# Optimization experiments

Measured on AMD Instinct MI355X. Metric: run time of the kernel, lower is better.

Reference implementation:

```python
import jax, jax.numpy as jnp
import numpy as np

H, W = 512, 1024            # panorama resolution
GRID = 512                  # occupancy histogram resolution (height=width=512)
ABS_SCALE = 20000.0         # mm, ground-plane extent
UNIT_SCALE = 1000.0         # m -> mm
COUNT_TH = 100.0            # histogram count clamp


def _xyz_sphere(ref_plan):
    # Vectorized version of the original double loop.
    i = np.arange(H, dtype=np.float32)
    j = np.arange(W, dtype=np.float32)
    theta = -np.pi * (i / (H - 1) - 0.5)          # [H]
    phi = np.pi * (2.0 * j / (W - 1) - 1.0)       # [W]
    ct, st = np.cos(theta)[:, None], np.sin(theta)[:, None]   # [H,1]
    cp, sp = np.cos(phi)[None, :], np.sin(phi)[None, :]       # [1,W]
    if ref_plan == 'horizontal':
        P = np.stack([cp * ct, sp * ct, np.broadcast_to(st, (H, W))], 0)
    elif ref_plan == 'vertical':
        P = np.stack([cp * ct, np.broadcast_to(-st, (H, W)), sp * ct], 0)
    else:  # lateral
        P = np.stack([sp * ct, np.broadcast_to(-st, (H, W)), cp * ct], 0)
    return jnp.asarray(P.astype(np.float32))      # [3,H,W]

_SPHERES = [_xyz_sphere(p) for p in ('horizontal', 'vertical', 'lateral')]


def _density_one(depth_hw, sph):
    # depth_hw: [H,W]; sph: [3,H,W]
    ps = depth_hw[None] * sph                               # [3,H,W] 3D points
    xy = ps[:2].reshape(2, -1) * UNIT_SCALE                 # [2,N] mm, (x,y)
    coords = (xy + ABS_SCALE / 2.0) / ABS_SCALE * GRID      # [2,N] in grid units
    coords = jnp.clip(jnp.round(coords), 0.0, GRID - 1).astype(jnp.int32)
    flat = coords[1] * GRID + coords[0]                     # density[y, x]
    hist = jnp.zeros(GRID * GRID, jnp.float32).at[flat].add(1.0)
    hist = jnp.minimum(hist, COUNT_TH)
    hist = hist / jnp.max(hist)
    return hist.reshape(GRID, GRID)


def _density(depth, sph):
    # depth: [B,1,H,W] -> [B,GRID,GRID], batched scatter histogram
    return jax.vmap(_density_one, in_axes=(0, None))(depth[:, 0], sph)


def _inverse_huber(pred, gt):
    # berHu loss: L1 below c = 0.2*max|d|, scaled L2 above.
    diff = jnp.abs(pred - gt)
    c = 0.2 * jnp.max(diff)
    loss = jnp.where(diff <= c, diff, (diff * diff + c * c) / (2.0 * c))
    return jnp.mean(loss)


def setup_inputs() -> dict:
    key = jax.random.key(0)
    k1, k2 = jax.random.split(key)
    # indoor depths in [0, 10) meters so histogram bins are populated
    pred = jax.random.uniform(k1, (16, 1, H, W), jnp.float32) * 10.0
    gt = jax.random.uniform(k2, (16, 1, H, W), jnp.float32) * 10.0
    return {"pred_depth": pred, "gt_depth": gt}


def reference(pred_depth, gt_depth):
    total = jnp.float32(0.0)
    for sph in _SPHERES:  # fixed 3 projection planes
        pred_om = _density(pred_depth, sph)
        gt_om = _density(gt_depth, sph)
        total = total + _inverse_huber(pred_om, gt_om)
    return total
```

## Files before the change

### kernel.cpp

```cpp
#include <hip/hip_runtime.h>

#define PI_F 3.14159265358979323846f

#define MAXZ_OFF_B   24576
#define HIST_OFF_B   32768
#define BUCK_OFF_B   25198592
#define REGION_U16   12320

__device__ inline float div20000(float a) {
    const float r = 1.0f / 20000.0f;
    float q0 = a * r;
    float e = fmaf(-20000.0f, q0, a);
    return fmaf(e, r, q0);
}

__device__ inline int bin1(float v) {
    float f = rintf(div20000(v + 10000.0f) * 512.0f);
    return (int)fminf(fmaxf(f, 0.0f), 511.0f);
}

__global__ __launch_bounds__(256) void bin_kernel(
    const float* __restrict__ pred, const float* __restrict__ gt,
    unsigned short* __restrict__ buck, unsigned* __restrict__ maxz,
    float* __restrict__ out) {
    __shared__ float sct[4], sst[4];
    __shared__ unsigned cnt[192];
    __shared__ unsigned bsum[24];
    __shared__ unsigned off[25];
    __shared__ __align__(16) unsigned short sdata[12288];
    const int tid = threadIdx.x, wg = blockIdx.x;
    const unsigned rep = (unsigned)(tid & 7);
    const int xcd = wg & 7, i4 = (wg >> 3) & 127, hh = wg >> 10;
    const int h = (hh << 3) | xcd;
    if (wg == 0) {
        if (tid < 128) maxz[tid] = 0u;
        if (tid == 128) out[0] = 0.0f;
    }
    if (tid < 192) cnt[tid] = 0u;
    if (tid < 4) {
        float fi = (float)(i4 * 4 + tid);
        float theta = -PI_F * (fi / 511.0f - 0.5f);
        sct[tid] = cosf(theta);
        sst[tid] = sinf(theta);
    }
    float cp[4], sp[4];
    #pragma unroll
    for (int k = 0; k < 4; ++k) {
        float fj = (float)(tid * 4 + k);
        float phi = PI_F * ((2.0f * fj) / 1023.0f - 1.0f);
        cp[k] = cosf(phi);
        sp[k] = sinf(phi);
    }
    __syncthreads();
    const float* img = ((h >> 4) ? gt : pred) + ((h & 15) << 19);
    unsigned items[48];
    #pragma unroll
    for (int r = 0; r < 4; ++r) {
        const int i = i4 * 4 + r;
        const float4 d4 = *(const float4*)(img + (i << 10) + (tid << 2));
        const float ct = sct[r], st = sst[r];
        #pragma unroll
        for (int k = 0; k < 4; ++k) {
            float d = (&d4.x)[k];
            float aA = cp[k] * ct;
            float aB = sp[k] * ct;
            float A = (d * aA) * 1000.0f;
            float B = (d * aB) * 1000.0f;
            float C = (d * (-st)) * 1000.0f;
            int iA = bin1(A), iB = bin1(B), iC = bin1(C);
            unsigned b0 = (unsigned)(iB >> 6);
            unsigned b1 = 8u + (unsigned)(iC >> 6);
            unsigned b2 = 16u + (unsigned)(iC >> 6);
            unsigned id0 = ((unsigned)(iB & 63) << 9) | (unsigned)iA;
            unsigned id1 = ((unsigned)(iC & 63) << 9) | (unsigned)iA;
            unsigned id2 = ((unsigned)(iC & 63) << 9) | (unsigned)iB;
            unsigned r0 = atomicAdd(&cnt[(b0 << 3) | rep], 1u);
            unsigned r1 = atomicAdd(&cnt[(b1 << 3) | rep], 1u);
            unsigned r2 = atomicAdd(&cnt[(b2 << 3) | rep], 1u);
            const int base = (r * 4 + k) * 3;
            items[base + 0] = (b0 << 27) | (rep << 24) | (r0 << 15) | id0;
            items[base + 1] = (b1 << 27) | (rep << 24) | (r1 << 15) | id1;
            items[base + 2] = (b2 << 27) | (rep << 24) | (r2 << 15) | id2;
        }
    }
    __syncthreads();
    if (tid < 24) {
        unsigned s = 0;
        #pragma unroll
        for (int r = 0; r < 8; ++r) {
            unsigned t = cnt[(tid << 3) | r];
            cnt[(tid << 3) | r] = s;
            s += t;
        }
        bsum[tid] = s;
    }
    __syncthreads();
    if (tid == 0) {
        unsigned s = 0;
        #pragma unroll
        for (int b = 0; b < 24; ++b) { off[b] = s; s += bsum[b]; }
        off[24] = s;
    }
    __syncthreads();
    if (tid < 24) {
        unsigned o = off[tid];
        #pragma unroll
        for (int r = 0; r < 8; ++r) cnt[(tid << 3) | r] += o;
    }
    __syncthreads();
    #pragma unroll
    for (int t = 0; t < 48; ++t) {
        const unsigned it = items[t];
        const unsigned slot = (it >> 27) * 8u + ((it >> 24) & 7u);
        sdata[cnt[slot] + ((it >> 15) & 511u)] = (unsigned short)(it & 32767u);
    }
    __syncthreads();
    unsigned short* regG = buck + (size_t)wg * REGION_U16;
    if (tid < 25) regG[tid] = (unsigned short)off[tid];
    const uint4* s4p = (const uint4*)sdata;
    uint4* g4 = (uint4*)(regG + 32);
    #pragma unroll
    for (int c = 0; c < 6; ++c) g4[(c << 8) + tid] = s4p[(c << 8) + tid];
}

__global__ __launch_bounds__(1024, 8) void scan_kernel(
    const unsigned short* __restrict__ buck, unsigned* __restrict__ hp,
    unsigned* __restrict__ maxraw) {
    __shared__ unsigned lh[16384];
    __shared__ unsigned s4[16];
    const int tid = threadIdx.x, wg = blockIdx.x;
    const int xcd = wg & 7, hhi = (wg >> 3) & 3;
    const int X = wg >> 5;
    const int pair = X / 6, idx6 = X % 6;
    const int plane = idx6 >> 1;
    const int band = (idx6 & 1) ? (4 + pair) : (3 - pair);
    const int h = (hhi << 3) | xcd;
    const int bucket = plane * 8 + band;

    #pragma unroll
    for (int k = 0; k < 4; ++k)
        *(uint4*)&lh[(k << 12) + (tid << 2)] = make_uint4(0, 0, 0, 0);
    __syncthreads();

    const int wid = tid >> 6, lane = tid & 63;
    for (int i4 = wid; i4 < 128; i4 += 16) {
        const unsigned short* reg =
            buck + (size_t)(xcd | (i4 << 3) | (hhi << 10)) * REGION_U16;
        const int lo = reg[bucket], hi = reg[bucket + 1];
        const unsigned short* data = reg + 32;
        int a = (lo + 7) & ~7;
        if (a > hi) a = hi;
        const int head = a - lo;
        if (lane < head) {
            const unsigned id = data[lo + lane];
            atomicAdd(&lh[id >> 1], 1u << ((id & 1u) << 4));
        }
        const int nv = (hi - a) >> 3;
        for (int v = lane; v < nv; v += 64) {
            const uint4 w = *(const uint4*)&data[a + (v << 3)];
            #pragma unroll
            for (int q = 0; q < 4; ++q) {
                const unsigned u = (&w.x)[q];
                const unsigned idl = u & 65535u, idh = u >> 16;
                atomicAdd(&lh[idl >> 1], 1u << ((idl & 1u) << 4));
                atomicAdd(&lh[idh >> 1], 1u << ((idh & 1u) << 4));
            }
        }
        const int tail = (hi - a) & 7;
        if (lane < tail) {
            const unsigned id = data[a + (nv << 3) + lane];
            atomicAdd(&lh[id >> 1], 1u << ((id & 1u) << 4));
        }
    }
    __syncthreads();

    unsigned m = 0;
    unsigned* gout = hp + ((plane * 32 + h) << 16) + (band << 13);
    #pragma unroll
    for (int k = 0; k < 8; ++k) {
        int w = (k << 10) + tid;
        unsigned v0 = lh[2 * w], v1 = lh[2 * w + 1];
        unsigned c0 = v0 & 65535u, c1 = v0 >> 16;
        unsigned c2 = v1 & 65535u, c3 = v1 >> 16;
        m = max(max(m, max(c0, c1)), max(c2, c3));
        gout[w] = min(c0, 255u) | (min(c1, 255u) << 8) |
                  (min(c2, 255u) << 16) | (min(c3, 255u) << 24);
    }
    #pragma unroll
    for (int o = 32; o; o >>= 1) m = max(m, (unsigned)__shfl_down((int)m, o));
    if ((tid & 63) == 0) s4[tid >> 6] = m;
    __syncthreads();
    if (tid == 0) {
        #pragma unroll
        for (int k = 1; k < 16; ++k) m = max(m, s4[k]);
        atomicMax(&maxraw[plane * 32 + h], m);
    }
}

__device__ inline float blockMaxF(float v) {
    #pragma unroll
    for (int o = 32; o; o >>= 1) v = fmaxf(v, __shfl_down(v, o));
    __shared__ float s[4];
    if ((threadIdx.x & 63) == 0) s[threadIdx.x >> 6] = v;
    __syncthreads();
    if (threadIdx.x == 0) v = fmaxf(fmaxf(s[0], s[1]), fmaxf(s[2], s[3]));
    return v;
}

__device__ inline float blockSumF(float v) {
    #pragma unroll
    for (int o = 32; o; o >>= 1) v += __shfl_down(v, o);
    __shared__ float s[4];
    if ((threadIdx.x & 63) == 0) s[threadIdx.x >> 6] = v;
    __syncthreads();
    if (threadIdx.x == 0) v = (s[0] + s[1]) + (s[2] + s[3]);
    return v;
}

__global__ void maxdiff_kernel(const unsigned* __restrict__ hp,
                               const unsigned* __restrict__ maxraw,
                               unsigned* __restrict__ maxdiff) {
    int blk = blockIdx.x;
    int b = blk & 15, chunk = (blk >> 4) & 15, plane = blk >> 8;
    const unsigned* P = hp + ((plane * 32 + b) << 16) + (chunk << 12);
    const unsigned* G = P + (16 << 16);
    float nP = fminf((float)maxraw[plane * 32 + b], 100.0f);
    float nG = fminf((float)maxraw[plane * 32 + 16 + b], 100.0f);
    float m = 0.0f;
    #pragma unroll
    for (int k = 0; k < 4; ++k) {
        uint4 wp = *(const uint4*)&P[(k << 10) + (threadIdx.x << 2)];
        uint4 wg = *(const uint4*)&G[(k << 10) + (threadIdx.x << 2)];
        #pragma unroll
        for (int w = 0; w < 4; ++w) {
            unsigned up = (&wp.x)[w], ug = (&wg.x)[w];
            #pragma unroll
            for (int s = 0; s < 32; s += 8) {
                float pn = fminf((float)((up >> s) & 255u), 100.0f) / nP;
                float gn = fminf((float)((ug >> s) & 255u), 100.0f) / nG;
                m = fmaxf(m, fabsf(pn - gn));
            }
        }
    }
    m = blockMaxF(m);
    if (threadIdx.x == 0) atomicMax(&maxdiff[plane], __float_as_uint(m));
}

__global__ void loss_kernel(const unsigned* __restrict__ hp,
                            const unsigned* __restrict__ maxraw,
                            const unsigned* __restrict__ maxdiff,
                            float* __restrict__ out) {
    int blk = blockIdx.x;
    int b = blk & 15, chunk = (blk >> 4) & 15, plane = blk >> 8;
    const unsigned* P = hp + ((plane * 32 + b) << 16) + (chunk << 12);
    const unsigned* G = P + (16 << 16);
    float c = 0.2f * __uint_as_float(maxdiff[plane]);
    float nP = fminf((float)maxraw[plane * 32 + b], 100.0f);
    float nG = fminf((float)maxraw[plane * 32 + 16 + b], 100.0f);
    float acc = 0.0f;
    #pragma unroll
    for (int k = 0; k < 4; ++k) {
        uint4 wp = *(const uint4*)&P[(k << 10) + (threadIdx.x << 2)];
        uint4 wg = *(const uint4*)&G[(k << 10) + (threadIdx.x << 2)];
        #pragma unroll
        for (int w = 0; w < 4; ++w) {
            unsigned up = (&wp.x)[w], ug = (&wg.x)[w];
            #pragma unroll
            for (int s = 0; s < 32; s += 8) {
                float pn = fminf((float)((up >> s) & 255u), 100.0f) / nP;
                float gn = fminf((float)((ug >> s) & 255u), 100.0f) / nG;
                float d = fabsf(pn - gn);
                acc += (d <= c) ? d : (d * d + c * c) / (2.0f * c);
            }
        }
    }
    acc = blockSumF(acc);
    if (threadIdx.x == 0) atomicAdd(out, acc / 4194304.0f);
}

extern "C" void kernel_launch(void* const* d_in, const int* in_sizes, int n_in,
                              void* d_out, int out_size, void* d_ws, size_t ws_size,
                              hipStream_t stream) {
    const float* pred = (const float*)d_in[0];
    const float* gt   = (const float*)d_in[1];
    float* out        = (float*)d_out;
    char* ws          = (char*)d_ws;

    unsigned* maxz    = (unsigned*)(ws + MAXZ_OFF_B);
    unsigned* maxraw  = maxz;
    unsigned* maxdiff = maxz + 96;
    unsigned* hp      = (unsigned*)(ws + HIST_OFF_B);
    unsigned short* buck = (unsigned short*)(ws + BUCK_OFF_B);

    bin_kernel<<<4096, 256, 0, stream>>>(pred, gt, buck, maxz, out);
    scan_kernel<<<768, 1024, 0, stream>>>(buck, hp, maxraw);
    maxdiff_kernel<<<768, 256, 0, stream>>>(hp, maxraw, maxdiff);
    loss_kernel<<<768, 256, 0, stream>>>(hp, maxraw, maxdiff, out);
}
```

Before: 211.0 us.

## Precompute trig tables, widen bucket counter replicas, run-length merge scan atomics

Adds a small trig_kernel that computes the cos/sin tables for phi and theta once into workspace and zeroes the accumulators. bin_kernel then loads these tables with vector reads instead of evaluating cosf/sinf per workgroup. The shared bucket counters go from 8 to 32 replicas to cut LDS atomic contention, and the item packing changes to match. The scan kernel now merges consecutive equal ids within each uint4 before issuing LDS atomics, which saves atomics when ids repeat at the cost of more branching. The extra kernel launch adds a small fixed overhead.

```diff
diff --git a/kernel.cpp b/kernel.cpp
--- a/kernel.cpp
+++ b/kernel.cpp
@@ -19,38 +19,45 @@
     return (int)fminf(fmaxf(f, 0.0f), 511.0f);
 }
 
+__global__ __launch_bounds__(256) void trig_kernel(
+    float* __restrict__ tbl, unsigned* __restrict__ maxz,
+    float* __restrict__ out) {
+    const int t = threadIdx.x + blockIdx.x * 256;
+    if (blockIdx.x == 0) {
+        if (threadIdx.x < 128) maxz[threadIdx.x] = 0u;
+        if (threadIdx.x == 128) out[0] = 0.0f;
+    }
+    if (t < 1024) {
+        float fj = (float)t;
+        float phi = PI_F * ((2.0f * fj) / 1023.0f - 1.0f);
+        tbl[t] = cosf(phi);
+        tbl[1024 + t] = sinf(phi);
+    } else {
+        int i = t - 1024;
+        float fi = (float)i;
+        float theta = -PI_F * (fi / 511.0f - 0.5f);
+        tbl[2048 + i] = cosf(theta);
+        tbl[2560 + i] = sinf(theta);
+    }
+}
+
 __global__ __launch_bounds__(256) void bin_kernel(
     const float* __restrict__ pred, const float* __restrict__ gt,
-    unsigned short* __restrict__ buck, unsigned* __restrict__ maxz,
-    float* __restrict__ out) {
-    __shared__ float sct[4], sst[4];
-    __shared__ unsigned cnt[192];
+    const float* __restrict__ tbl, unsigned short* __restrict__ buck) {
+    __shared__ unsigned cnt[768];
     __shared__ unsigned bsum[24];
     __shared__ unsigned off[25];
     __shared__ __align__(16) unsigned short sdata[12288];
     const int tid = threadIdx.x, wg = blockIdx.x;
-    const unsigned rep = (unsigned)(tid & 7);
+    const unsigned rep = (unsigned)(tid & 31);
     const int xcd = wg & 7, i4 = (wg >> 3) & 127, hh = wg >> 10;
     const int h = (hh << 3) | xcd;
-    if (wg == 0) {
-        if (tid < 128) maxz[tid] = 0u;
-        if (tid == 128) out[0] = 0.0f;
-    }
-    if (tid < 192) cnt[tid] = 0u;
-    if (tid < 4) {
-        float fi = (float)(i4 * 4 + tid);
-        float theta = -PI_F * (fi / 511.0f - 0.5f);
-        sct[tid] = cosf(theta);
-        sst[tid] = sinf(theta);
-    }
-    float cp[4], sp[4];
-    #pragma unroll
-    for (int k = 0; k < 4; ++k) {
-        float fj = (float)(tid * 4 + k);
-        float phi = PI_F * ((2.0f * fj) / 1023.0f - 1.0f);
-        cp[k] = cosf(phi);
-        sp[k] = sinf(phi);
-    }
+    #pragma unroll
+    for (int z = 0; z < 3; ++z) cnt[tid + (z << 8)] = 0u;
+    const float4 cp4 = *(const float4*)&tbl[tid << 2];
+    const float4 sp4 = *(const float4*)&tbl[1024 + (tid << 2)];
+    const float4 ct4 = *(const float4*)&tbl[2048 + (i4 << 2)];
+    const float4 st4 = *(const float4*)&tbl[2560 + (i4 << 2)];
     __syncthreads();
     const float* img = ((h >> 4) ? gt : pred) + ((h & 15) << 19);
     unsigned items[48];
@@ -58,38 +65,38 @@
     for (int r = 0; r < 4; ++r) {
         const int i = i4 * 4 + r;
         const float4 d4 = *(const float4*)(img + (i << 10) + (tid << 2));
-        const float ct = sct[r], st = sst[r];
+        const float ct = (&ct4.x)[r], st = (&st4.x)[r];
         #pragma unroll
         for (int k = 0; k < 4; ++k) {
             float d = (&d4.x)[k];
-            float aA = cp[k] * ct;
-            float aB = sp[k] * ct;
+            float aA = (&cp4.x)[k] * ct;
+            float aB = (&sp4.x)[k] * ct;
             float A = (d * aA) * 1000.0f;
             float B = (d * aB) * 1000.0f;
             float C = (d * (-st)) * 1000.0f;
             int iA = bin1(A), iB = bin1(B), iC = bin1(C);
-            unsigned b0 = (unsigned)(iB >> 6);
-            unsigned b1 = 8u + (unsigned)(iC >> 6);
-            unsigned b2 = 16u + (unsigned)(iC >> 6);
-            unsigned id0 = ((unsigned)(iB & 63) << 9) | (unsigned)iA;
-            unsigned id1 = ((unsigned)(iC & 63) << 9) | (unsigned)iA;
-            unsigned id2 = ((unsigned)(iC & 63) << 9) | (unsigned)iB;
-            unsigned r0 = atomicAdd(&cnt[(b0 << 3) | rep], 1u);
-            unsigned r1 = atomicAdd(&cnt[(b1 << 3) | rep], 1u);
-            unsigned r2 = atomicAdd(&cnt[(b2 << 3) | rep], 1u);
+            unsigned f0 = ((unsigned)iB << 9) | (unsigned)iA;
+            unsigned f1 = ((unsigned)iC << 9) | (unsigned)iA;
+            unsigned f2 = ((unsigned)iC << 9) | (unsigned)iB;
+            unsigned b0 = f0 >> 15;
+            unsigned b1 = 8u + (f1 >> 15);
+            unsigned b2 = 16u + (f2 >> 15);
+            unsigned r0 = atomicAdd(&cnt[(b0 << 5) | rep], 1u);
+            unsigned r1 = atomicAdd(&cnt[(b1 << 5) | rep], 1u);
+            unsigned r2 = atomicAdd(&cnt[(b2 << 5) | rep], 1u);
             const int base = (r * 4 + k) * 3;
-            items[base + 0] = (b0 << 27) | (rep << 24) | (r0 << 15) | id0;
-            items[base + 1] = (b1 << 27) | (rep << 24) | (r1 << 15) | id1;
-            items[base + 2] = (b2 << 27) | (rep << 24) | (r2 << 15) | id2;
+            items[base + 0] = (b0 << 27) | (rep << 22) | (r0 << 15) | (f0 & 32767u);
+            items[base + 1] = (b1 << 27) | (rep << 22) | (r1 << 15) | (f1 & 32767u);
+            items[base + 2] = (b2 << 27) | (rep << 22) | (r2 << 15) | (f2 & 32767u);
         }
     }
     __syncthreads();
     if (tid < 24) {
         unsigned s = 0;
         #pragma unroll
-        for (int r = 0; r < 8; ++r) {
-            unsigned t = cnt[(tid << 3) | r];
-            cnt[(tid << 3) | r] = s;
+        for (int r = 0; r < 32; ++r) {
+            unsigned t = cnt[(tid << 5) | r];
+            cnt[(tid << 5) | r] = s;
             s += t;
         }
         bsum[tid] = s;
@@ -105,14 +112,14 @@
     if (tid < 24) {
         unsigned o = off[tid];
         #pragma unroll
-        for (int r = 0; r < 8; ++r) cnt[(tid << 3) | r] += o;
+        for (int r = 0; r < 32; ++r) cnt[(tid << 5) | r] += o;
     }
     __syncthreads();
     #pragma unroll
     for (int t = 0; t < 48; ++t) {
         const unsigned it = items[t];
-        const unsigned slot = (it >> 27) * 8u + ((it >> 24) & 7u);
-        sdata[cnt[slot] + ((it >> 15) & 511u)] = (unsigned short)(it & 32767u);
+        const unsigned slot = ((it >> 27) << 5) | ((it >> 22) & 31u);
+        sdata[cnt[slot] + ((it >> 15) & 127u)] = (unsigned short)(it & 32767u);
     }
     __syncthreads();
     unsigned short* regG = buck + (size_t)wg * REGION_U16;
@@ -158,13 +165,19 @@
         const int nv = (hi - a) >> 3;
         for (int v = lane; v < nv; v += 64) {
             const uint4 w = *(const uint4*)&data[a + (v << 3)];
-            #pragma unroll
-            for (int q = 0; q < 4; ++q) {
-                const unsigned u = (&w.x)[q];
-                const unsigned idl = u & 65535u, idh = u >> 16;
-                atomicAdd(&lh[idl >> 1], 1u << ((idl & 1u) << 4));
-                atomicAdd(&lh[idh >> 1], 1u << ((idh & 1u) << 4));
-            }
+            unsigned prev = w.x & 65535u, c = 1;
+            auto step = [&](unsigned id) {
+                if (id == prev) { ++c; }
+                else {
+                    atomicAdd(&lh[prev >> 1], c << ((prev & 1u) << 4));
+                    prev = id; c = 1;
+                }
+            };
+            step(w.x >> 16);
+            step(w.y & 65535u); step(w.y >> 16);
+            step(w.z & 65535u); step(w.z >> 16);
+            step(w.w & 65535u); step(w.w >> 16);
+            atomicAdd(&lh[prev >> 1], c << ((prev & 1u) << 4));
         }
         const int tail = (hi - a) & 7;
         if (lane < tail) {
@@ -286,13 +299,15 @@
     float* out        = (float*)d_out;
     char* ws          = (char*)d_ws;
 
+    float* tbl        = (float*)ws;
     unsigned* maxz    = (unsigned*)(ws + MAXZ_OFF_B);
     unsigned* maxraw  = maxz;
     unsigned* maxdiff = maxz + 96;
     unsigned* hp      = (unsigned*)(ws + HIST_OFF_B);
     unsigned short* buck = (unsigned short*)(ws + BUCK_OFF_B);
 
-    bin_kernel<<<4096, 256, 0, stream>>>(pred, gt, buck, maxz, out);
+    trig_kernel<<<6, 256, 0, stream>>>(tbl, maxz, out);
+    bin_kernel<<<4096, 256, 0, stream>>>(pred, gt, tbl, buck);
     scan_kernel<<<768, 1024, 0, stream>>>(buck, hp, maxraw);
     maxdiff_kernel<<<768, 256, 0, stream>>>(hp, maxraw, maxdiff);
     loss_kernel<<<768, 256, 0, stream>>>(hp, maxraw, maxdiff, out);
```

Result: slower. 215.7 us (+2.2%).
